# Optimization experiments

Measured on AMD Instinct MI355X. Metric: run time of the kernel, lower is better.

The kernel has to match this reference:

```python
import jax, jax.numpy as jnp
import numpy as np

N_QUBITS = 12
RANK = 1024
K = 4            # outcomes per qubit
D = 2 ** N_QUBITS
N_IDX = 1_000_000


def setup_inputs() -> dict:
    key = jax.random.key(0)
    k1, k2, k3, k4 = jax.random.split(key, 4)
    params = jax.random.normal(k1, (2, D, RANK), dtype=jnp.float32)
    M_real = jax.random.normal(k2, (K, 2, 2), dtype=jnp.float32)
    M_imag = jax.random.normal(k3, (K, 2, 2), dtype=jnp.float32)
    P_idxs = jax.random.randint(k4, (N_IDX,), 0, K ** N_QUBITS, dtype=jnp.int64)
    return {"params": params, "M_real": M_real, "M_imag": M_imag, "P_idxs": P_idxs}


def _qmt(rho, M, n_qubits):
    """Born rule: P[s1..sN] = Tr[(M_{s1} x ... x M_{sN}) rho].
    Sequential per-qubit contraction; T has shape [K^n, 2^(N-n), 2^(N-n)]."""
    T = rho[None, :, :]  # axes: (done outcomes, row legs j, col legs i)
    for _ in range(n_qubits):
        k, r, c = T.shape[0], T.shape[1] // 2, T.shape[2] // 2
        Tt = T.reshape(k, 2, r, 2, c)  # (k, j_n, j_rest, i_n, i_rest)
        # Tr contribution: sum_{i,j} M[s,i,j] * rho[j,i]
        T = jnp.einsum('sij,kjait->ksat', M, Tt).reshape(k * M.shape[0], r, c)
    return T.reshape(-1)  # [K^N] complex


def reference(params, M_real, M_imag, P_idxs):
    # rho = U U^H / Tr(U U^H)
    U = jax.lax.complex(params[0], params[1])            # [D, RANK] complex64
    rho = U @ U.conj().T                                  # [D, D]
    rho = rho / jnp.trace(rho)
    M = jax.lax.complex(M_real, M_imag)                   # [K, 2, 2] complex64
    P_all = _qmt(rho, M, N_QUBITS).real                   # [K^N] float32
    return P_all[P_idxs]
```

## Files before the change

kernel.cpp:

```cpp
#include <hip/hip_runtime.h>

#define D 4096
#define RANK 1024
#define UELEMS 4194304ULL
#define NTOT 16777216ULL
#define QSCALE 16000.0f

typedef __attribute__((ext_vector_type(4))) int i32x4;

__device__ float g_inv_tr[1];
__device__ float g_scale[D];
__device__ float g_mdre[16];
__device__ float g_mdim[16];

static __device__ __forceinline__ void load_lds16(const void* g, void* l) {
    __builtin_amdgcn_global_load_lds(
        (const __attribute__((address_space(1))) unsigned int*)g,
        (__attribute__((address_space(3))) unsigned int*)l, 16, 0, 0);
}

#define MFMA_I8 __builtin_amdgcn_mfma_i32_16x16x64_i8

__global__ __launch_bounds__(256) void convert_w_i8(const float* __restrict__ P,
                                                    const float* __restrict__ Mre,
                                                    const float* __restrict__ Mim,
                                                    char* __restrict__ Wh,
                                                    char* __restrict__ Wl)
{
    if (blockIdx.x == 0 && threadIdx.x < 16) {
        const int s = threadIdx.x >> 2, i = (threadIdx.x >> 1) & 1, j = threadIdx.x & 1;
        g_mdre[threadIdx.x] =  Mre[s * 4 + j * 2 + i];
        g_mdim[threadIdx.x] = -Mim[s * 4 + j * 2 + i];
    }

    const int w = threadIdx.x >> 6, lane = threadIdx.x & 63;
    const int row = blockIdx.x * 4 + w;

    float ur[16], ui[16];
    const float* pr = P + (size_t)row * RANK + lane * 16;
    const float* pi = P + UELEMS + (size_t)row * RANK + lane * 16;
    #pragma unroll
    for (int q = 0; q < 4; ++q) {
        const float4 a = ((const float4*)pr)[q];
        const float4 b = ((const float4*)pi)[q];
        ur[q * 4 + 0] = a.x; ur[q * 4 + 1] = a.y; ur[q * 4 + 2] = a.z; ur[q * 4 + 3] = a.w;
        ui[q * 4 + 0] = b.x; ui[q * 4 + 1] = b.y; ui[q * 4 + 2] = b.z; ui[q * 4 + 3] = b.w;
    }
    float mx = 0.f;
    #pragma unroll
    for (int e = 0; e < 16; ++e)
        mx = fmaxf(mx, fmaxf(fabsf(ur[e]), fabsf(ui[e])));
    #pragma unroll
    for (int off = 1; off < 64; off <<= 1)
        mx = fmaxf(mx, __shfl_xor(mx, off));
    const float inv = mx > 0.f ? QSCALE / mx : 0.f;
    if (lane == 0) g_scale[row] = mx / QSCALE;

    int hr[16], lr[16], hi[16], li[16];
    #pragma unroll
    for (int e = 0; e < 16; ++e) {
        float q = ur[e] * inv;
        float hf = rintf(q * 0.0078125f);
        hr[e] = (int)hf; lr[e] = (int)rintf(q - 128.f * hf);
        q = ui[e] * inv;
        hf = rintf(q * 0.0078125f);
        hi[e] = (int)hf; li[e] = (int)rintf(q - 128.f * hf);
    }
    uint4 phr, plr, phi, pli;
    unsigned* dst[4] = {(unsigned*)&phr, (unsigned*)&plr, (unsigned*)&phi, (unsigned*)&pli};
    #pragma unroll
    for (int q = 0; q < 4; ++q) {
        unsigned a = 0, b = 0, c = 0, d = 0;
        #pragma unroll
        for (int k = 0; k < 4; ++k) {
            const int sh = k * 8;
            a |= (unsigned)(hr[q * 4 + k] & 255) << sh;
            b |= (unsigned)(lr[q * 4 + k] & 255) << sh;
            c |= (unsigned)(hi[q * 4 + k] & 255) << sh;
            d |= (unsigned)(li[q * 4 + k] & 255) << sh;
        }
        dst[0][q] = a; dst[1][q] = b; dst[2][q] = c; dst[3][q] = d;
    }
    const size_t b1 = (size_t)row * 2048 + lane * 16;
    *(uint4*)&Wh[b1] = phr;          *(uint4*)&Wl[b1] = plr;
    *(uint4*)&Wh[b1 + 1024] = phi;   *(uint4*)&Wl[b1 + 1024] = pli;
}

__global__ __launch_bounds__(512, 2) void gemm_rho_i8(const char* __restrict__ Wh,
                                                      const char* __restrict__ Wl,
                                                      float2* __restrict__ rho)
{
    __shared__ __align__(16) char sA[2][4][128 * 64];
    __shared__ __align__(16) char sB[2][4][64 * 64];

    const int g = blockIdx.x;
    int bi = (int)((sqrtf(4.f * (float)g + 1.f) - 1.f) * 0.5f);
    while (bi > 0 && bi * (bi + 1) > g) --bi;
    while ((bi + 1) * (bi + 2) <= g) ++bi;
    const int bj = g - bi * (bi + 1);
    const int row0 = bi << 7, col0 = bj << 6;

    const int t = threadIdx.x;
    const int lane = t & 63, w = t >> 6;
    const int wr = w >> 1, wc = w & 1;

    const int ra = t >> 2;
    const int kca = (t & 3) ^ ((ra >> 1) & 3);
    const size_t aoff = (size_t)(row0 + ra) * 2048 + kca * 16;
    const int ldsAo = t * 16;
    const int tb = t & 255;
    const int rb = tb >> 2;
    const int kcb = (t & 3) ^ ((rb >> 1) & 3);
    const int hiw = (t >= 256) ? 1 : 0;
    const size_t boff = (size_t)(col0 + rb) * 2048 + kcb * 16 + hiw * 1024;
    const int ldsB0o = hiw * 8192 + tb * 16;
    const int ldsB1o = ldsB0o + 4096;

    const int m = lane & 15, gq = lane >> 4;
    const int fko = (gq ^ ((m >> 1) & 3)) * 16;

    i32x4 rehh[2][2], remx[2][2], iphh[2][2], ipmx[2][2], iqhh[2][2], iqmx[2][2];
    #pragma unroll
    for (int i = 0; i < 2; ++i)
        #pragma unroll
        for (int j = 0; j < 2; ++j) {
            rehh[i][j] = (i32x4){0, 0, 0, 0}; remx[i][j] = (i32x4){0, 0, 0, 0};
            iphh[i][j] = (i32x4){0, 0, 0, 0}; ipmx[i][j] = (i32x4){0, 0, 0, 0};
            iqhh[i][j] = (i32x4){0, 0, 0, 0}; iqmx[i][j] = (i32x4){0, 0, 0, 0};
        }

    char* const sA0 = &sA[0][0][0];
    char* const sB0 = &sB[0][0][0];

    load_lds16(Wh + aoff,        sA0 + ldsAo);
    load_lds16(Wl + aoff,        sA0 + 8192  + ldsAo);
    load_lds16(Wh + aoff + 1024, sA0 + 16384 + ldsAo);
    load_lds16(Wl + aoff + 1024, sA0 + 24576 + ldsAo);
    load_lds16(Wh + boff,        sB0 + ldsB0o);
    load_lds16(Wl + boff,        sB0 + ldsB1o);
    __syncthreads();

#define DO_MFMA_J(j)                                                          \
    _Pragma("unroll")                                                         \
    for (int i = 0; i < 2; ++i) {                                             \
        i32x4 r;                                                              \
        r = rehh[i][j];                                                       \
        r = MFMA_I8(fa1h[i], b1h, r, 0, 0, 0);                                \
        r = MFMA_I8(fa2h[i], b2h, r, 0, 0, 0);                                \
        rehh[i][j] = r;                                                       \
        r = remx[i][j];                                                       \
        r = MFMA_I8(fa1h[i], b1l, r, 0, 0, 0);                                \
        r = MFMA_I8(fa1l[i], b1h, r, 0, 0, 0);                                \
        r = MFMA_I8(fa2h[i], b2l, r, 0, 0, 0);                                \
        r = MFMA_I8(fa2l[i], b2h, r, 0, 0, 0);                                \
        remx[i][j] = r;                                                       \
        r = MFMA_I8(fa2h[i], b1h, iphh[i][j], 0, 0, 0); iphh[i][j] = r;       \
        r = ipmx[i][j];                                                       \
        r = MFMA_I8(fa2h[i], b1l, r, 0, 0, 0);                                \
        r = MFMA_I8(fa2l[i], b1h, r, 0, 0, 0);                                \
        ipmx[i][j] = r;                                                       \
        r = MFMA_I8(fa1h[i], b2h, iqhh[i][j], 0, 0, 0); iqhh[i][j] = r;       \
        r = iqmx[i][j];                                                       \
        r = MFMA_I8(fa1h[i], b2l, r, 0, 0, 0);                                \
        r = MFMA_I8(fa1l[i], b2h, r, 0, 0, 0);                                \
        iqmx[i][j] = r;                                                       \
    }

    #pragma unroll 2
    for (int kt = 0; kt < 16; ++kt) {
        const int cur = kt & 1;
        const char* sAc = sA0 + cur * 32768;
        const char* sBc = sB0 + cur * 16384;
        char* sAn = sA0 + (cur ^ 1) * 32768;
        char* sBn = sB0 + (cur ^ 1) * 16384;
        const size_t ko = (size_t)(kt + 1) * 64;

        i32x4 fa1h[2], fa1l[2], fa2h[2], fa2l[2];
        i32x4 b1h, b1l, b2h, b2l;

        #pragma unroll
        for (int i = 0; i < 2; ++i) {
            const int off = (wr * 32 + i * 16 + m) * 64 + fko;
            fa1h[i] = *(const i32x4*)(sAc + off);
            fa1l[i] = *(const i32x4*)(sAc + 8192  + off);
            fa2h[i] = *(const i32x4*)(sAc + 16384 + off);
            fa2l[i] = *(const i32x4*)(sAc + 24576 + off);
        }
        {
            const int off = (wc * 32 + m) * 64 + fko;
            b1h = *(const i32x4*)(sBc + off);
            b1l = *(const i32x4*)(sBc + 4096  + off);
            b2h = *(const i32x4*)(sBc + 8192  + off);
            b2l = *(const i32x4*)(sBc + 12288 + off);
        }
        if (kt < 15) {
            load_lds16(Wh + aoff + ko,        sAn + ldsAo);
            load_lds16(Wl + aoff + ko,        sAn + 8192  + ldsAo);
            load_lds16(Wh + aoff + ko + 1024, sAn + 16384 + ldsAo);
            load_lds16(Wl + aoff + ko + 1024, sAn + 24576 + ldsAo);
        }
        __builtin_amdgcn_s_barrier();
        asm volatile("s_waitcnt lgkmcnt(0)" ::: "memory");
        __builtin_amdgcn_sched_barrier(0);
        __builtin_amdgcn_s_setprio(1);
        DO_MFMA_J(0)
        __builtin_amdgcn_s_setprio(0);
        __builtin_amdgcn_s_barrier();

        {
            const int off = (wc * 32 + 16 + m) * 64 + fko;
            b1h = *(const i32x4*)(sBc + off);
            b1l = *(const i32x4*)(sBc + 4096  + off);
            b2h = *(const i32x4*)(sBc + 8192  + off);
            b2l = *(const i32x4*)(sBc + 12288 + off);
        }
        if (kt < 15) {
            load_lds16(Wh + boff + ko, sBn + ldsB0o);
            load_lds16(Wl + boff + ko, sBn + ldsB1o);
        }
        __builtin_amdgcn_s_barrier();
        asm volatile("s_waitcnt lgkmcnt(0)" ::: "memory");
        __builtin_amdgcn_sched_barrier(0);
        __builtin_amdgcn_s_setprio(1);
        DO_MFMA_J(1)
        __builtin_amdgcn_s_setprio(0);

        __syncthreads();
    }
#undef DO_MFMA_J

    #pragma unroll
    for (int j = 0; j < 2; ++j) {
        const int col = col0 + wc * 32 + j * 16 + m;
        const float sc = g_scale[col];
        const int c64 = col >> 6;
        #pragma unroll
        for (int i = 0; i < 2; ++i) {
            #pragma unroll
            for (int r = 0; r < 4; ++r) {
                const int row = row0 + wr * 32 + i * 16 + gq * 4 + r;
                const float s2 = g_scale[row] * sc;
                const float re = s2 * (16384.f * (float)rehh[i][j][r] + 128.f * (float)remx[i][j][r]);
                const float im = s2 * (16384.f * (float)(iphh[i][j][r] - iqhh[i][j][r])
                                      + 128.f * (float)(ipmx[i][j][r] - iqmx[i][j][r]));
                const int r64 = row >> 6;
                if (r64 > c64 || row >= col) rho[(size_t)row * D + col] = make_float2(re, im);
                if (r64 == c64 && row > col) rho[(size_t)col * D + row] = make_float2(re, -im);
            }
        }
    }
}

__global__ void trace_inv(const float2* __restrict__ rho)
{
    __shared__ float red[256];
    float s = 0.f;
    for (int d = threadIdx.x; d < D; d += 256)
        s += rho[(size_t)d * (D + 1)].x;
    red[threadIdx.x] = s;
    __syncthreads();
    for (int off = 128; off > 0; off >>= 1) {
        if (threadIdx.x < off) red[threadIdx.x] += red[threadIdx.x + off];
        __syncthreads();
    }
    if (threadIdx.x == 0) g_inv_tr[0] = 1.0f / red[0];
}

static __device__ __forceinline__ void qmt2(float2* x,
                                            const float* __restrict__ Mre,
                                            const float* __restrict__ Mim)
{
    float2 y[16];
    #pragma unroll
    for (int sb = 0; sb < 4; ++sb)
        #pragma unroll
        for (int ja = 0; ja < 2; ++ja)
            #pragma unroll
            for (int ia = 0; ia < 2; ++ia) {
                float2 acc = make_float2(0.f, 0.f);
                #pragma unroll
                for (int ib = 0; ib < 2; ++ib)
                    #pragma unroll
                    for (int jb = 0; jb < 2; ++jb) {
                        const float mr = Mre[sb * 4 + ib * 2 + jb];
                        const float mi = Mim[sb * 4 + ib * 2 + jb];
                        const float2 v = x[(ja * 2 + jb) * 4 + ia * 2 + ib];
                        acc.x += mr * v.x - mi * v.y;
                        acc.y += mr * v.y + mi * v.x;
                    }
                y[sb * 4 + ja * 2 + ia] = acc;
            }
    #pragma unroll
    for (int sa = 0; sa < 4; ++sa)
        #pragma unroll
        for (int sb = 0; sb < 4; ++sb) {
            float2 acc = make_float2(0.f, 0.f);
            #pragma unroll
            for (int ia = 0; ia < 2; ++ia)
                #pragma unroll
                for (int ja = 0; ja < 2; ++ja) {
                    const float mr = Mre[sa * 4 + ia * 2 + ja];
                    const float mi = Mim[sa * 4 + ia * 2 + ja];
                    const float2 v = y[sb * 4 + ja * 2 + ia];
                    acc.x += mr * v.x - mi * v.y;
                    acc.y += mr * v.y + mi * v.x;
                }
            x[sa * 4 + sb] = acc;
        }
}

static __device__ __forceinline__ void pA_pipeline(float2* x, float2* X, const int t,
                                                   const float* __restrict__ mre,
                                                   const float* __restrict__ mim)
{
    qmt2(x, mre, mim);
    #pragma unroll
    for (int d = 0; d < 16; ++d) X[t * 17 + d] = x[d];
    __syncthreads();
    const int a2 = t >> 6, t2 = (t >> 4) & 3, d1 = t & 15;
    #pragma unroll
    for (int j2 = 0; j2 < 4; ++j2)
        #pragma unroll
        for (int i2 = 0; i2 < 4; ++i2)
            x[j2 * 4 + i2] = X[((a2 * 4 + j2) * 16 + t2 * 4 + i2) * 17 + d1];
    __syncthreads();
    qmt2(x, mre, mim);
    #pragma unroll
    for (int d = 0; d < 16; ++d) X[(a2 * 4 + t2) * 257 + d * 16 + d1] = x[d];
    __syncthreads();
    const int e2 = t >> 4, e1 = t & 15;
    #pragma unroll
    for (int j2 = 0; j2 < 4; ++j2)
        #pragma unroll
        for (int i2 = 0; i2 < 4; ++i2)
            x[j2 * 4 + i2] = X[(j2 * 4 + i2) * 257 + e2 * 16 + e1];
    qmt2(x, mre, mim);
}

__global__ __launch_bounds__(256) void qmt_pAh(const float2* __restrict__ in,
                                               float2* __restrict__ out,
                                               const float* __restrict__ Mre,
                                               const float* __restrict__ Mim)
{
    __shared__ __align__(16) float2 X[256 * 17];
    const int t = threadIdx.x;
    const int g = blockIdx.x;
    int rr = (int)((sqrtf(8.f * (float)g + 1.f) - 1.f) * 0.5f);
    while (rr * (rr + 1) / 2 > g) --rr;
    while ((rr + 1) * (rr + 2) / 2 <= g) ++rr;
    const int cc = g - rr * (rr + 1) / 2;

    const int a4 = t >> 4, t4 = t & 15;
    float2 x0[16], x[16];
    #pragma unroll
    for (int j2 = 0; j2 < 4; ++j2) {
        const float2* p = in + ((size_t)(rr * 64 + a4 * 4 + j2)) * 4096 + cc * 64 + t4 * 4;
        const float4 v0 = ((const float4*)p)[0];
        const float4 v1 = ((const float4*)p)[1];
        x0[j2 * 4 + 0] = make_float2(v0.x, v0.y);
        x0[j2 * 4 + 1] = make_float2(v0.z, v0.w);
        x0[j2 * 4 + 2] = make_float2(v1.x, v1.y);
        x0[j2 * 4 + 3] = make_float2(v1.z, v1.w);
    }

    #pragma unroll
    for (int q = 0; q < 16; ++q) x[q] = x0[q];
    pA_pipeline(x, X, t, Mre, Mim);
    const int e2 = t >> 4, e1 = t & 15;
    const size_t ob0 = (size_t)(rr * 64 + cc) * 4096 + e2 * 16 + e1;
    #pragma unroll
    for (int d = 0; d < 16; ++d) out[ob0 + (size_t)d * 256] = x[d];

    if (rr != cc) {
        __syncthreads();
        #pragma unroll
        for (int q = 0; q < 16; ++q) x[q] = x0[q];
        pA_pipeline(x, X, t, g_mdre, g_mdim);
        const size_t ob1 = (size_t)(cc * 64 + rr) * 4096 + e2 * 16 + e1;
        #pragma unroll
        for (int d = 0; d < 16; ++d)
            out[ob1 + (size_t)d * 256] = make_float2(x[d].x, -x[d].y);
    }
}

static __device__ __forceinline__ void qmt_stage_cb_half(float2* x,
                                                         const float* __restrict__ Mre,
                                                         const float* __restrict__ Mim)
{
    #pragma unroll
    for (int jb = 0; jb < 2; ++jb) {
        float2 y[16];
        #pragma unroll
        for (int sc = 0; sc < 4; ++sc)
            #pragma unroll
            for (int ii = 0; ii < 4; ++ii) {
                float2 acc = make_float2(0.f, 0.f);
                #pragma unroll
                for (int ic = 0; ic < 2; ++ic)
                    #pragma unroll
                    for (int jc = 0; jc < 2; ++jc) {
                        const float mr = Mre[sc * 4 + ic * 2 + jc];
                        const float mi = Mim[sc * 4 + ic * 2 + jc];
                        const float2 v = x[jb * 16 + jc * 8 + ii * 2 + ic];
                        acc.x += mr * v.x - mi * v.y;
                        acc.y += mr * v.y + mi * v.x;
                    }
                y[sc * 4 + ii] = acc;
            }
        #pragma unroll
        for (int q = 0; q < 16; ++q) x[jb * 16 + q] = y[q];
    }
    #pragma unroll
    for (int sc = 0; sc < 4; ++sc) {
        float2 z[8];
        #pragma unroll
        for (int sb = 0; sb < 4; ++sb)
            #pragma unroll
            for (int ia = 0; ia < 2; ++ia) {
                float2 acc = make_float2(0.f, 0.f);
                #pragma unroll
                for (int ib = 0; ib < 2; ++ib)
                    #pragma unroll
                    for (int jb = 0; jb < 2; ++jb) {
                        const float mr = Mre[sb * 4 + ib * 2 + jb];
                        const float mi = Mim[sb * 4 + ib * 2 + jb];
                        const float2 v = x[jb * 16 + sc * 4 + ia * 2 + ib];
                        acc.x += mr * v.x - mi * v.y;
                        acc.y += mr * v.y + mi * v.x;
                    }
                z[sb * 2 + ia] = acc;
            }
        #pragma unroll
        for (int sb = 0; sb < 4; ++sb)
            #pragma unroll
            for (int ia = 0; ia < 2; ++ia)
                x[(sb >> 1) * 16 + sc * 4 + ia * 2 + (sb & 1)] = z[sb * 2 + ia];
    }
}

#define STAGE_A_COEFFS                                                        \
    float Are[2][2], Aim[2][2], Bre[2][2], Bim[2][2];                         \
    _Pragma("unroll")                                                         \
    for (int sal = 0; sal < 2; ++sal)                                         \
        _Pragma("unroll")                                                     \
        for (int ia = 0; ia < 2; ++ia) {                                      \
            const int sa = 2 * h + sal;                                       \
            Are[sal][ia] = Mre[sa * 4 + ia * 2 + h];                          \
            Aim[sal][ia] = Mim[sa * 4 + ia * 2 + h];                          \
            Bre[sal][ia] = Mre[sa * 4 + ia * 2 + (1 - h)];                    \
            Bim[sal][ia] = Mim[sa * 4 + ia * 2 + (1 - h)];                    \
        }

__global__ __launch_bounds__(256) void qmt_p3(const float2* __restrict__ in,
                                              float2* __restrict__ out,
                                              const float* __restrict__ Mre,
                                              const float* __restrict__ Mim)
{
    const int t = threadIdx.x;
    const int h = (t >> 5) & 1;
    const int idx = blockIdx.x * 4 + (t >> 6);
    const int rc = idx >> 7;
    const int r3 = rc >> 3, c3 = rc & 7;
    const int s = (idx & 127) * 32 + (t & 31);

    float2 x[32];
    #pragma unroll
    for (int jb = 0; jb < 2; ++jb)
        #pragma unroll
        for (int jc = 0; jc < 2; ++jc) {
            const int j3 = 4 * h + 2 * jb + jc;
            #pragma unroll
            for (int i3 = 0; i3 < 8; ++i3)
                x[jb * 16 + jc * 8 + i3] =
                    in[(size_t)((r3 * 8 + j3) * 64 + c3 * 8 + i3) * 4096 + s];
        }

    qmt_stage_cb_half(x, Mre, Mim);

    STAGE_A_COEFFS
    const size_t ob = ((size_t)(r3 * 8 + c3) * 64) * 4096 + s;
    #pragma unroll
    for (int sbH = 0; sbH < 2; ++sbH)
        #pragma unroll
        for (int sc = 0; sc < 4; ++sc)
            #pragma unroll
            for (int sbL = 0; sbL < 2; ++sbL) {
                const int q = sbH * 16 + sc * 4 + sbL;
                const float2 o0 = x[q], o1 = x[q + 2];
                float2 r0, r1;
                r0.x = __shfl_xor(o0.x, 32); r0.y = __shfl_xor(o0.y, 32);
                r1.x = __shfl_xor(o1.x, 32); r1.y = __shfl_xor(o1.y, 32);
                const int sb = sbH * 2 + sbL;
                #pragma unroll
                for (int sal = 0; sal < 2; ++sal) {
                    const float re = Are[sal][0] * o0.x - Aim[sal][0] * o0.y
                                   + Are[sal][1] * o1.x - Aim[sal][1] * o1.y
                                   + Bre[sal][0] * r0.x - Bim[sal][0] * r0.y
                                   + Bre[sal][1] * r1.x - Bim[sal][1] * r1.y;
                    const float im = Are[sal][0] * o0.y + Aim[sal][0] * o0.x
                                   + Are[sal][1] * o1.y + Aim[sal][1] * o1.x
                                   + Bre[sal][0] * r0.y + Bim[sal][0] * r0.x
                                   + Bre[sal][1] * r1.y + Bim[sal][1] * r1.x;
                    const int s3 = (2 * h + sal) * 16 + sb * 4 + sc;
                    out[ob + (size_t)s3 * 4096] = make_float2(re, im);
                }
            }
}

__global__ __launch_bounds__(256) void qmt_p4(const float2* __restrict__ in,
                                              float* __restrict__ out,
                                              const float* __restrict__ Mre,
                                              const float* __restrict__ Mim)
{
    const int t = threadIdx.x;
    const int h = (t >> 5) & 1;
    const int s = (blockIdx.x * 4 + (t >> 6)) * 32 + (t & 31);

    float2 x[32];
    #pragma unroll
    for (int jb = 0; jb < 2; ++jb)
        #pragma unroll
        for (int jc = 0; jc < 2; ++jc) {
            const int j3 = 4 * h + 2 * jb + jc;
            #pragma unroll
            for (int i3 = 0; i3 < 8; ++i3)
                x[jb * 16 + jc * 8 + i3] = in[(size_t)(j3 * 8 + i3) * 262144 + s];
        }

    qmt_stage_cb_half(x, Mre, Mim);

    STAGE_A_COEFFS
    const size_t ob = (size_t)(s >> 5) * 2048 + (s & 31);
    #pragma unroll
    for (int sbH = 0; sbH < 2; ++sbH)
        #pragma unroll
        for (int sc = 0; sc < 4; ++sc)
            #pragma unroll
            for (int sbL = 0; sbL < 2; ++sbL) {
                const int q = sbH * 16 + sc * 4 + sbL;
                const float2 o0 = x[q], o1 = x[q + 2];
                float2 r0, r1;
                r0.x = __shfl_xor(o0.x, 32); r0.y = __shfl_xor(o0.y, 32);
                r1.x = __shfl_xor(o1.x, 32); r1.y = __shfl_xor(o1.y, 32);
                const int sb = sbH * 2 + sbL;
                #pragma unroll
                for (int sal = 0; sal < 2; ++sal) {
                    const float re = Are[sal][0] * o0.x - Aim[sal][0] * o0.y
                                   + Are[sal][1] * o1.x - Aim[sal][1] * o1.y
                                   + Bre[sal][0] * r0.x - Bim[sal][0] * r0.y
                                   + Bre[sal][1] * r1.x - Bim[sal][1] * r1.y;
                    const int s3 = (2 * h + sal) * 16 + sb * 4 + sc;
                    out[ob + (size_t)s3 * 32] = re;
                }
            }
}

__global__ void gather_idx(const float* __restrict__ P, const int* __restrict__ idxs,
                           float* __restrict__ out, const int n)
{
    const int i = blockIdx.x * 256 + threadIdx.x;
    if (i < n) {
        const int idx = idxs[i];
        const int s = idx & 262143;
        const size_t pos = (size_t)(s >> 5) * 2048 + (size_t)(idx >> 18) * 32 + (s & 31);
        out[i] = P[pos] * g_inv_tr[0];
    }
}

extern "C" void kernel_launch(void* const* d_in, const int* in_sizes, int n_in,
                              void* d_out, int out_size, void* d_ws, size_t ws_size,
                              hipStream_t stream)
{
    const float* params = (const float*)d_in[0];
    const float* Mre    = (const float*)d_in[1];
    const float* Mim    = (const float*)d_in[2];
    const int*   idxs   = (const int*)d_in[3];
    float*       out    = (float*)d_out;

    float* ws = (float*)d_ws;
    float2* A  = (float2*)ws;
    float2* Bp = (float2*)(ws + 2 * NTOT);
    char* Wh = (char*)Bp;
    char* Wl = Wh + (size_t)D * 2048;

    convert_w_i8<<<1024, 256, 0, stream>>>(params, Mre, Mim, Wh, Wl);
    gemm_rho_i8<<<1056, 512, 0, stream>>>(Wh, Wl, A);
    trace_inv<<<1, 256, 0, stream>>>(A);

    qmt_pAh<<<2080, 256, 0, stream>>>(A, Bp, Mre, Mim);
    qmt_p3<<<2048, 256, 0, stream>>>(Bp, A, Mre, Mim);
    qmt_p4<<<2048, 256, 0, stream>>>(A, (float*)Bp, Mre, Mim);

    gather_idx<<<(out_size + 255) / 256, 256, 0, stream>>>((float*)Bp, idxs, out, out_size);
}
```

Before: 395.9 us.

## Restructure GEMM k-loop barriers and vectorize QMT stages to two elements per thread

The int8 GEMM k-loop now issues all next-tile LDS prefetches at the top and loads both B fragments at once. It drops the two mid-iteration barriers, so the MFMA groups for both column halves run back to back. Separately, qmt_p3 and qmt_p4 now process two adjacent elements per thread with float4 loads and stores, which halves their grid sizes. This aims to cut barrier stalls in the GEMM and memory-transaction overhead in the QMT passes, at the cost of higher register pressure and possibly weaker load/compute overlap.

```diff
diff --git a/kernel.cpp b/kernel.cpp
--- a/kernel.cpp
+++ b/kernel.cpp
@@ -145,24 +145,24 @@
     for (int i = 0; i < 2; ++i) {                                             \
         i32x4 r;                                                              \
         r = rehh[i][j];                                                       \
-        r = MFMA_I8(fa1h[i], b1h, r, 0, 0, 0);                                \
-        r = MFMA_I8(fa2h[i], b2h, r, 0, 0, 0);                                \
+        r = MFMA_I8(fa1h[i], b1h[j], r, 0, 0, 0);                             \
+        r = MFMA_I8(fa2h[i], b2h[j], r, 0, 0, 0);                             \
         rehh[i][j] = r;                                                       \
         r = remx[i][j];                                                       \
-        r = MFMA_I8(fa1h[i], b1l, r, 0, 0, 0);                                \
-        r = MFMA_I8(fa1l[i], b1h, r, 0, 0, 0);                                \
-        r = MFMA_I8(fa2h[i], b2l, r, 0, 0, 0);                                \
-        r = MFMA_I8(fa2l[i], b2h, r, 0, 0, 0);                                \
+        r = MFMA_I8(fa1h[i], b1l[j], r, 0, 0, 0);                             \
+        r = MFMA_I8(fa1l[i], b1h[j], r, 0, 0, 0);                             \
+        r = MFMA_I8(fa2h[i], b2l[j], r, 0, 0, 0);                             \
+        r = MFMA_I8(fa2l[i], b2h[j], r, 0, 0, 0);                             \
         remx[i][j] = r;                                                       \
-        r = MFMA_I8(fa2h[i], b1h, iphh[i][j], 0, 0, 0); iphh[i][j] = r;       \
+        r = MFMA_I8(fa2h[i], b1h[j], iphh[i][j], 0, 0, 0); iphh[i][j] = r;    \
         r = ipmx[i][j];                                                       \
-        r = MFMA_I8(fa2h[i], b1l, r, 0, 0, 0);                                \
-        r = MFMA_I8(fa2l[i], b1h, r, 0, 0, 0);                                \
+        r = MFMA_I8(fa2h[i], b1l[j], r, 0, 0, 0);                             \
+        r = MFMA_I8(fa2l[i], b1h[j], r, 0, 0, 0);                             \
         ipmx[i][j] = r;                                                       \
-        r = MFMA_I8(fa1h[i], b2h, iqhh[i][j], 0, 0, 0); iqhh[i][j] = r;       \
+        r = MFMA_I8(fa1h[i], b2h[j], iqhh[i][j], 0, 0, 0); iqhh[i][j] = r;    \
         r = iqmx[i][j];                                                       \
-        r = MFMA_I8(fa1h[i], b2l, r, 0, 0, 0);                                \
-        r = MFMA_I8(fa1l[i], b2h, r, 0, 0, 0);                                \
+        r = MFMA_I8(fa1h[i], b2l[j], r, 0, 0, 0);                             \
+        r = MFMA_I8(fa1l[i], b2h[j], r, 0, 0, 0);                             \
         iqmx[i][j] = r;                                                       \
     }
 
@@ -175,9 +175,17 @@
         char* sBn = sB0 + (cur ^ 1) * 16384;
         const size_t ko = (size_t)(kt + 1) * 64;
 
+        if (kt < 15) {
+            load_lds16(Wh + aoff + ko,        sAn + ldsAo);
+            load_lds16(Wl + aoff + ko,        sAn + 8192  + ldsAo);
+            load_lds16(Wh + aoff + ko + 1024, sAn + 16384 + ldsAo);
+            load_lds16(Wl + aoff + ko + 1024, sAn + 24576 + ldsAo);
+            load_lds16(Wh + boff + ko, sBn + ldsB0o);
+            load_lds16(Wl + boff + ko, sBn + ldsB1o);
+        }
+
         i32x4 fa1h[2], fa1l[2], fa2h[2], fa2l[2];
-        i32x4 b1h, b1l, b2h, b2l;
-
+        i32x4 b1h[2], b1l[2], b2h[2], b2l[2];
         #pragma unroll
         for (int i = 0; i < 2; ++i) {
             const int off = (wr * 32 + i * 16 + m) * 64 + fko;
@@ -186,42 +194,17 @@
             fa2h[i] = *(const i32x4*)(sAc + 16384 + off);
             fa2l[i] = *(const i32x4*)(sAc + 24576 + off);
         }
-        {
-            const int off = (wc * 32 + m) * 64 + fko;
-            b1h = *(const i32x4*)(sBc + off);
-            b1l = *(const i32x4*)(sBc + 4096  + off);
-            b2h = *(const i32x4*)(sBc + 8192  + off);
-            b2l = *(const i32x4*)(sBc + 12288 + off);
-        }
-        if (kt < 15) {
-            load_lds16(Wh + aoff + ko,        sAn + ldsAo);
-            load_lds16(Wl + aoff + ko,        sAn + 8192  + ldsAo);
-            load_lds16(Wh + aoff + ko + 1024, sAn + 16384 + ldsAo);
-            load_lds16(Wl + aoff + ko + 1024, sAn + 24576 + ldsAo);
-        }
-        __builtin_amdgcn_s_barrier();
-        asm volatile("s_waitcnt lgkmcnt(0)" ::: "memory");
-        __builtin_amdgcn_sched_barrier(0);
+        #pragma unroll
+        for (int j = 0; j < 2; ++j) {
+            const int off = (wc * 32 + j * 16 + m) * 64 + fko;
+            b1h[j] = *(const i32x4*)(sBc + off);
+            b1l[j] = *(const i32x4*)(sBc + 4096  + off);
+            b2h[j] = *(const i32x4*)(sBc + 8192  + off);
+            b2l[j] = *(const i32x4*)(sBc + 12288 + off);
+        }
+
         __builtin_amdgcn_s_setprio(1);
         DO_MFMA_J(0)
-        __builtin_amdgcn_s_setprio(0);
-        __builtin_amdgcn_s_barrier();
-
-        {
-            const int off = (wc * 32 + 16 + m) * 64 + fko;
-            b1h = *(const i32x4*)(sBc + off);
-            b1l = *(const i32x4*)(sBc + 4096  + off);
-            b2h = *(const i32x4*)(sBc + 8192  + off);
-            b2l = *(const i32x4*)(sBc + 12288 + off);
-        }
-        if (kt < 15) {
-            load_lds16(Wh + boff + ko, sBn + ldsB0o);
-            load_lds16(Wl + boff + ko, sBn + ldsB1o);
-        }
-        __builtin_amdgcn_s_barrier();
-        asm volatile("s_waitcnt lgkmcnt(0)" ::: "memory");
-        __builtin_amdgcn_sched_barrier(0);
-        __builtin_amdgcn_s_setprio(1);
         DO_MFMA_J(1)
         __builtin_amdgcn_s_setprio(0);
 
@@ -383,28 +366,33 @@
     }
 }
 
-static __device__ __forceinline__ void qmt_stage_cb_half(float2* x,
-                                                         const float* __restrict__ Mre,
-                                                         const float* __restrict__ Mim)
+static __device__ __forceinline__ void cmacc4(float4& a, const float mr, const float mi,
+                                              const float4 v)
+{
+    a.x += mr * v.x - mi * v.y;
+    a.y += mr * v.y + mi * v.x;
+    a.z += mr * v.z - mi * v.w;
+    a.w += mr * v.w + mi * v.z;
+}
+
+static __device__ __forceinline__ void qmt_stage_cb_half4(float4* x,
+                                                          const float* __restrict__ Mre,
+                                                          const float* __restrict__ Mim)
 {
     #pragma unroll
     for (int jb = 0; jb < 2; ++jb) {
-        float2 y[16];
+        float4 y[16];
         #pragma unroll
         for (int sc = 0; sc < 4; ++sc)
             #pragma unroll
             for (int ii = 0; ii < 4; ++ii) {
-                float2 acc = make_float2(0.f, 0.f);
+                float4 acc = make_float4(0.f, 0.f, 0.f, 0.f);
                 #pragma unroll
                 for (int ic = 0; ic < 2; ++ic)
                     #pragma unroll
-                    for (int jc = 0; jc < 2; ++jc) {
-                        const float mr = Mre[sc * 4 + ic * 2 + jc];
-                        const float mi = Mim[sc * 4 + ic * 2 + jc];
-                        const float2 v = x[jb * 16 + jc * 8 + ii * 2 + ic];
-                        acc.x += mr * v.x - mi * v.y;
-                        acc.y += mr * v.y + mi * v.x;
-                    }
+                    for (int jc = 0; jc < 2; ++jc)
+                        cmacc4(acc, Mre[sc * 4 + ic * 2 + jc], Mim[sc * 4 + ic * 2 + jc],
+                               x[jb * 16 + jc * 8 + ii * 2 + ic]);
                 y[sc * 4 + ii] = acc;
             }
         #pragma unroll
@@ -412,22 +400,18 @@
     }
     #pragma unroll
     for (int sc = 0; sc < 4; ++sc) {
-        float2 z[8];
+        float4 z[8];
         #pragma unroll
         for (int sb = 0; sb < 4; ++sb)
             #pragma unroll
             for (int ia = 0; ia < 2; ++ia) {
-                float2 acc = make_float2(0.f, 0.f);
+                float4 acc = make_float4(0.f, 0.f, 0.f, 0.f);
                 #pragma unroll
                 for (int ib = 0; ib < 2; ++ib)
                     #pragma unroll
-                    for (int jb = 0; jb < 2; ++jb) {
-                        const float mr = Mre[sb * 4 + ib * 2 + jb];
-                        const float mi = Mim[sb * 4 + ib * 2 + jb];
-                        const float2 v = x[jb * 16 + sc * 4 + ia * 2 + ib];
-                        acc.x += mr * v.x - mi * v.y;
-                        acc.y += mr * v.y + mi * v.x;
-                    }
+                    for (int jb = 0; jb < 2; ++jb)
+                        cmacc4(acc, Mre[sb * 4 + ib * 2 + jb], Mim[sb * 4 + ib * 2 + jb],
+                               x[jb * 16 + sc * 4 + ia * 2 + ib]);
                 z[sb * 2 + ia] = acc;
             }
         #pragma unroll
@@ -451,6 +435,10 @@
             Bim[sal][ia] = Mim[sa * 4 + ia * 2 + (1 - h)];                    \
         }
 
+#define SHFL4(dst, src)                                                       \
+    dst.x = __shfl_xor(src.x, 32); dst.y = __shfl_xor(src.y, 32);             \
+    dst.z = __shfl_xor(src.z, 32); dst.w = __shfl_xor(src.w, 32);
+
 __global__ __launch_bounds__(256) void qmt_p3(const float2* __restrict__ in,
                                               float2* __restrict__ out,
                                               const float* __restrict__ Mre,
@@ -459,11 +447,11 @@
     const int t = threadIdx.x;
     const int h = (t >> 5) & 1;
     const int idx = blockIdx.x * 4 + (t >> 6);
-    const int rc = idx >> 7;
+    const int rc = idx >> 6;
     const int r3 = rc >> 3, c3 = rc & 7;
-    const int s = (idx & 127) * 32 + (t & 31);
-
-    float2 x[32];
+    const int s = ((idx & 63) * 32 + (t & 31)) * 2;
+
+    float4 x[32];
     #pragma unroll
     for (int jb = 0; jb < 2; ++jb)
         #pragma unroll
@@ -471,11 +459,11 @@
             const int j3 = 4 * h + 2 * jb + jc;
             #pragma unroll
             for (int i3 = 0; i3 < 8; ++i3)
-                x[jb * 16 + jc * 8 + i3] =
-                    in[(size_t)((r3 * 8 + j3) * 64 + c3 * 8 + i3) * 4096 + s];
-        }
-
-    qmt_stage_cb_half(x, Mre, Mim);
+                x[jb * 16 + jc * 8 + i3] = *(const float4*)
+                    &in[(size_t)((r3 * 8 + j3) * 64 + c3 * 8 + i3) * 4096 + s];
+        }
+
+    qmt_stage_cb_half4(x, Mre, Mim);
 
     STAGE_A_COEFFS
     const size_t ob = ((size_t)(r3 * 8 + c3) * 64) * 4096 + s;
@@ -486,23 +474,32 @@
             #pragma unroll
             for (int sbL = 0; sbL < 2; ++sbL) {
                 const int q = sbH * 16 + sc * 4 + sbL;
-                const float2 o0 = x[q], o1 = x[q + 2];
-                float2 r0, r1;
-                r0.x = __shfl_xor(o0.x, 32); r0.y = __shfl_xor(o0.y, 32);
-                r1.x = __shfl_xor(o1.x, 32); r1.y = __shfl_xor(o1.y, 32);
+                const float4 o0 = x[q], o1 = x[q + 2];
+                float4 r0, r1;
+                SHFL4(r0, o0)
+                SHFL4(r1, o1)
                 const int sb = sbH * 2 + sbL;
                 #pragma unroll
                 for (int sal = 0; sal < 2; ++sal) {
-                    const float re = Are[sal][0] * o0.x - Aim[sal][0] * o0.y
-                                   + Are[sal][1] * o1.x - Aim[sal][1] * o1.y
-                                   + Bre[sal][0] * r0.x - Bim[sal][0] * r0.y
-                                   + Bre[sal][1] * r1.x - Bim[sal][1] * r1.y;
-                    const float im = Are[sal][0] * o0.y + Aim[sal][0] * o0.x
-                                   + Are[sal][1] * o1.y + Aim[sal][1] * o1.x
-                                   + Bre[sal][0] * r0.y + Bim[sal][0] * r0.x
-                                   + Bre[sal][1] * r1.y + Bim[sal][1] * r1.x;
+                    float4 res;
+                    res.x = Are[sal][0] * o0.x - Aim[sal][0] * o0.y
+                          + Are[sal][1] * o1.x - Aim[sal][1] * o1.y
+                          + Bre[sal][0] * r0.x - Bim[sal][0] * r0.y
+                          + Bre[sal][1] * r1.x - Bim[sal][1] * r1.y;
+                    res.y = Are[sal][0] * o0.y + Aim[sal][0] * o0.x
+                          + Are[sal][1] * o1.y + Aim[sal][1] * o1.x
+                          + Bre[sal][0] * r0.y + Bim[sal][0] * r0.x
+                          + Bre[sal][1] * r1.y + Bim[sal][1] * r1.x;
+                    res.z = Are[sal][0] * o0.z - Aim[sal][0] * o0.w
+                          + Are[sal][1] * o1.z - Aim[sal][1] * o1.w
+                          + Bre[sal][0] * r0.z - Bim[sal][0] * r0.w
+                          + Bre[sal][1] * r1.z - Bim[sal][1] * r1.w;
+                    res.w = Are[sal][0] * o0.w + Aim[sal][0] * o0.z
+                          + Are[sal][1] * o1.w + Aim[sal][1] * o1.z
+                          + Bre[sal][0] * r0.w + Bim[sal][0] * r0.z
+                          + Bre[sal][1] * r1.w + Bim[sal][1] * r1.z;
                     const int s3 = (2 * h + sal) * 16 + sb * 4 + sc;
-                    out[ob + (size_t)s3 * 4096] = make_float2(re, im);
+                    *(float4*)&out[ob + (size_t)s3 * 4096] = res;
                 }
             }
 }
@@ -514,9 +511,9 @@
 {
     const int t = threadIdx.x;
     const int h = (t >> 5) & 1;
-    const int s = (blockIdx.x * 4 + (t >> 6)) * 32 + (t & 31);
-
-    float2 x[32];
+    const int s = ((blockIdx.x * 4 + (t >> 6)) * 32 + (t & 31)) * 2;
+
+    float4 x[32];
     #pragma unroll
     for (int jb = 0; jb < 2; ++jb)
         #pragma unroll
@@ -524,10 +521,11 @@
             const int j3 = 4 * h + 2 * jb + jc;
             #pragma unroll
             for (int i3 = 0; i3 < 8; ++i3)
-                x[jb * 16 + jc * 8 + i3] = in[(size_t)(j3 * 8 + i3) * 262144 + s];
-        }
-
-    qmt_stage_cb_half(x, Mre, Mim);
+                x[jb * 16 + jc * 8 + i3] = *(const float4*)
+                    &in[(size_t)(j3 * 8 + i3) * 262144 + s];
+        }
+
+    qmt_stage_cb_half4(x, Mre, Mim);
 
     STAGE_A_COEFFS
     const size_t ob = (size_t)(s >> 5) * 2048 + (s & 31);
@@ -538,19 +536,24 @@
             #pragma unroll
             for (int sbL = 0; sbL < 2; ++sbL) {
                 const int q = sbH * 16 + sc * 4 + sbL;
-                const float2 o0 = x[q], o1 = x[q + 2];
-                float2 r0, r1;
-                r0.x = __shfl_xor(o0.x, 32); r0.y = __shfl_xor(o0.y, 32);
-                r1.x = __shfl_xor(o1.x, 32); r1.y = __shfl_xor(o1.y, 32);
+                const float4 o0 = x[q], o1 = x[q + 2];
+                float4 r0, r1;
+                SHFL4(r0, o0)
+                SHFL4(r1, o1)
                 const int sb = sbH * 2 + sbL;
                 #pragma unroll
                 for (int sal = 0; sal < 2; ++sal) {
-                    const float re = Are[sal][0] * o0.x - Aim[sal][0] * o0.y
-                                   + Are[sal][1] * o1.x - Aim[sal][1] * o1.y
-                                   + Bre[sal][0] * r0.x - Bim[sal][0] * r0.y
-                                   + Bre[sal][1] * r1.x - Bim[sal][1] * r1.y;
+                    float2 res;
+                    res.x = Are[sal][0] * o0.x - Aim[sal][0] * o0.y
+                          + Are[sal][1] * o1.x - Aim[sal][1] * o1.y
+                          + Bre[sal][0] * r0.x - Bim[sal][0] * r0.y
+                          + Bre[sal][1] * r1.x - Bim[sal][1] * r1.y;
+                    res.y = Are[sal][0] * o0.z - Aim[sal][0] * o0.w
+                          + Are[sal][1] * o1.z - Aim[sal][1] * o1.w
+                          + Bre[sal][0] * r0.z - Bim[sal][0] * r0.w
+                          + Bre[sal][1] * r1.z - Bim[sal][1] * r1.w;
                     const int s3 = (2 * h + sal) * 16 + sb * 4 + sc;
-                    out[ob + (size_t)s3 * 32] = re;
+                    *(float2*)&out[ob + (size_t)s3 * 32] = res;
                 }
             }
 }
@@ -588,8 +591,8 @@
     trace_inv<<<1, 256, 0, stream>>>(A);
 
     qmt_pAh<<<2080, 256, 0, stream>>>(A, Bp, Mre, Mim);
-    qmt_p3<<<2048, 256, 0, stream>>>(Bp, A, Mre, Mim);
-    qmt_p4<<<2048, 256, 0, stream>>>(A, (float*)Bp, Mre, Mim);
+    qmt_p3<<<1024, 256, 0, stream>>>(Bp, A, Mre, Mim);
+    qmt_p4<<<1024, 256, 0, stream>>>(A, (float*)Bp, Mre, Mim);
 
     gather_idx<<<(out_size + 255) / 256, 256, 0, stream>>>((float*)Bp, idxs, out, out_size);
 }
```

Result: slower. 435.7 us (+10.0%).
